# Optimization experiments

Hardware: AMD Instinct MI355X
Metric: run time of the kernel (lower is better)

Reference implementation:

```python
import jax, jax.numpy as jnp
import numpy as np
from jax import lax

DIM = 192
HID = 768  # dim * mlp_ratio
B, H, W = 16, 64, 64


def setup_inputs() -> dict:
    key = jax.random.key(0)
    ks = jax.random.split(key, 20)
    n = lambda k, shape, s=0.05: jax.random.normal(k, shape, dtype=jnp.float32) * s
    return {
        "x": jax.random.normal(ks[0], (B, DIM, H, W), dtype=jnp.float32),
        "ln1_w": jnp.ones((DIM,), jnp.float32), "ln1_b": jnp.zeros((DIM,), jnp.float32),
        "in_proj_w": n(ks[1], (2 * DIM, DIM)), "in_proj_b": n(ks[2], (2 * DIM,)),
        "dw_k": n(ks[3], (DIM, 1, 3, 3)),
        "le_k": n(ks[4], (DIM, 1, 3, 3)),
        "decay_logits": n(ks[5], (4, DIM), 0.5),
        "mix_logits": n(ks[6], (4, DIM), 0.5),
        "input_scale": n(ks[7], (4, DIM), 0.5),
        "bn_w": jnp.ones((DIM,), jnp.float32), "bn_b": jnp.zeros((DIM,), jnp.float32),
        "out_proj_w": n(ks[8], (DIM, DIM)), "out_proj_b": n(ks[9], (DIM,)),
        "ln2_w": jnp.ones((DIM,), jnp.float32), "ln2_b": jnp.zeros((DIM,), jnp.float32),
        "fc1_w": n(ks[10], (HID, DIM)), "fc1_b": n(ks[11], (HID,)),
        "fc2_w": n(ks[12], (DIM, HID)), "fc2_b": n(ks[13], (DIM,)),
    }


def _ln2d(x, w, b, eps=1e-6):
    # LayerNorm over channel dim of NCHW
    mean = jnp.mean(x, axis=1, keepdims=True)
    var = jnp.mean((x - mean) ** 2, axis=1, keepdims=True)
    xn = (x - mean) / jnp.sqrt(var + eps)
    return xn * w[None, :, None, None] + b[None, :, None, None]


def _conv1x1(x, w, b):
    return jnp.einsum('bchw,oc->bohw', x, w) + b[None, :, None, None]


def _dwconv3(x, k):
    # depthwise 3x3, padding=1; k: (C,1,3,3)
    return lax.conv_general_dilated(x, k, (1, 1), 'SAME',
                                    feature_group_count=x.shape[1],
                                    dimension_numbers=('NCHW', 'OIHW', 'NCHW'))


def _scan_axis(x, decay, axis):
    # linear decay scan along `axis` (-1 width, -2 height)
    xs = jnp.moveaxis(x, axis, 0)  # (L, B, C, ...)
    d = decay[None, :, None]  # broadcast over (B, C, other_spatial)
    def step(s, cur):
        s = d * s + (1.0 - d) * cur
        return s, s
    _, ys = lax.scan(step, jnp.zeros_like(xs[0]), xs)
    return jnp.moveaxis(ys, 0, axis)


def _directional_scan(x, decay_logits, mix_logits, input_scale):
    decay = jnp.clip(jax.nn.sigmoid(decay_logits), 0.05, 0.995)  # (4,C)
    mix = jax.nn.softmax(mix_logits, axis=0)  # (4,C)
    iscale = 1.0 + jnp.tanh(input_scale)  # (4,C)
    sc = lambda a: a[:, None, None]  # (C,1,1) -> broadcast NCHW
    lr = _scan_axis(x * sc(iscale[0]), decay[0], -1)
    rl = jnp.flip(_scan_axis(jnp.flip(x, -1) * sc(iscale[1]), decay[1], -1), -1)
    tb = _scan_axis(x * sc(iscale[2]), decay[2], -2)
    bt = jnp.flip(_scan_axis(jnp.flip(x, -2) * sc(iscale[3]), decay[3], -2), -2)
    return sc(mix[0]) * lr + sc(mix[1]) * rl + sc(mix[2]) * tb + sc(mix[3]) * bt


def reference(x, ln1_w, ln1_b, in_proj_w, in_proj_b, dw_k, le_k,
              decay_logits, mix_logits, input_scale, bn_w, bn_b,
              out_proj_w, out_proj_b, ln2_w, ln2_b, fc1_w, fc1_b, fc2_w, fc2_b):
    # --- SSM branch ---
    h = _ln2d(x, ln1_w, ln1_b)
    pg = _conv1x1(h, in_proj_w, in_proj_b)
    projected, gate = jnp.split(pg, 2, axis=1)
    projected = _dwconv3(projected, dw_k)
    scanned = _directional_scan(projected, decay_logits, mix_logits, input_scale)
    local = _dwconv3(projected, le_k)
    mixed = (scanned + local) * jax.nn.sigmoid(gate)
    # BatchNorm2d (training-mode batch statistics, eps=1e-5)
    bmean = jnp.mean(mixed, axis=(0, 2, 3), keepdims=True)
    bvar = jnp.mean((mixed - bmean) ** 2, axis=(0, 2, 3), keepdims=True)
    bn = (mixed - bmean) / jnp.sqrt(bvar + 1e-5)
    bn = bn * bn_w[None, :, None, None] + bn_b[None, :, None, None]
    mixed = jax.nn.gelu(bn, approximate=False)
    x = x + _conv1x1(mixed, out_proj_w, out_proj_b)
    # --- MLP branch ---
    h2 = _ln2d(x, ln2_w, ln2_b)
    m = jax.nn.gelu(_conv1x1(h2, fc1_w, fc1_b), approximate=False)
    m = _conv1x1(m, fc2_w, fc2_b)
    return x + m
```

## Files before the change

### kernel.cpp

```cpp
#include <hip/hip_runtime.h>
#include <math.h>

#define CH 192
#define HW 4096
#define NB 16
#define NELEM (NB*CH*HW)
#define HIDN 768

typedef __bf16 bf16x8 __attribute__((ext_vector_type(8)));
typedef float  f32x4  __attribute__((ext_vector_type(4)));
typedef unsigned uint4v __attribute__((ext_vector_type(4)));

__device__ __forceinline__ float gelu_f(float v){
    return v / (1.0f + __expf(-1.702f*v));
}
__device__ __forceinline__ float sigmoid_f(float v){
    return 1.0f / (1.0f + __expf(-v));
}
__device__ __forceinline__ void gload16(const void* g, void* l){
    __builtin_amdgcn_global_load_lds(
        (const __attribute__((address_space(1))) unsigned*)g,
        (__attribute__((address_space(3))) unsigned*)l, 16, 0, 0);
}

__global__ __launch_bounds__(256) void k_cvt_all(
    const float* __restrict__ a0, const float* __restrict__ a1,
    const float* __restrict__ a2, const float* __restrict__ a3,
    __bf16* __restrict__ o)
{
    const int n0 = 2*CH*CH, n1 = CH*CH, n2 = HIDN*CH, n3 = CH*HIDN;
    int i = blockIdx.x*256 + threadIdx.x;
    if (i < n0) o[i] = (__bf16)a0[i];
    else if (i < n0+n1) o[i] = (__bf16)a1[i-n0];
    else if (i < n0+n1+n2) o[i] = (__bf16)a2[i-n0-n1];
    else if (i < n0+n1+n2+n3) o[i] = (__bf16)a3[i-n0-n1-n2];
}

__global__ __launch_bounds__(256, 4) void k_ln_inproj(
    const float* __restrict__ x, const float* __restrict__ lw, const float* __restrict__ lb,
    const __bf16* __restrict__ Wb, const float* __restrict__ bias,
    __bf16* __restrict__ proj, __bf16* __restrict__ gate)
{
    __shared__ __align__(16) unsigned char smem[33792];
    __bf16* h2s = (__bf16*)smem;
    float* redS = (float*)(smem + 24576);
    float* redQ = (float*)(smem + 25600);
    float* mS   = (float*)(smem + 26624);
    float* rS   = (float*)(smem + 26880);
    __bf16* outb = (__bf16*)(smem + 24576);

    int tid = threadIdx.x;
    int lane = tid & 63;
    int w = tid >> 6;
    int lo = lane & 15, hi = lane >> 4;
    int bid = blockIdx.x;
    int b = bid >> 6;
    int p0 = (bid & 63) << 6;
    const float* xb = x + (size_t)b*CH*HW + p0;
    int px = lane;

    float xv[48];
    float s = 0.f, s2 = 0.f;
    #pragma unroll
    for (int k = 0; k < 48; ++k){
        float v = xb[(size_t)(48*w + k)*HW + px];
        xv[k] = v; s += v; s2 += v*v;
    }
    redS[tid] = s; redQ[tid] = s2;
    __syncthreads();
    if (tid < 64){
        float S = redS[tid]+redS[tid+64]+redS[tid+128]+redS[tid+192];
        float Q = redQ[tid]+redQ[tid+64]+redQ[tid+128]+redQ[tid+192];
        float mean = S * (1.f/192.f);
        float var  = Q * (1.f/192.f) - mean*mean;
        mS[tid] = mean;
        rS[tid] = rsqrtf(var + 1e-6f);
    }
    __syncthreads();
    {
        float mean = mS[px], rstd = rS[px];
        #pragma unroll
        for (int m = 0; m < 6; ++m){
            int c8 = 48*w + 8*m;
            int ks = c8 >> 5, hh = (c8 >> 3) & 3;
            bf16x8 pk;
            #pragma unroll
            for (int j = 0; j < 8; ++j){
                int c = c8 + j;
                pk[j] = (__bf16)((xv[8*m + j] - mean) * rstd * lw[c] + lb[c]);
            }
            *(bf16x8*)(h2s + (((px>>4)*6 + ks)*64 + hh*16 + (px & 15))*8) = pk;
        }
    }
    __syncthreads();

    #pragma unroll
    for (int g = 0; g < 2; ++g){
        f32x4 acc[3][4];
        #pragma unroll
        for (int nt = 0; nt < 3; ++nt)
            #pragma unroll
            for (int pt = 0; pt < 4; ++pt)
                acc[nt][pt] = (f32x4){0.f,0.f,0.f,0.f};
        #pragma unroll
        for (int ks = 0; ks < 6; ++ks){
            bf16x8 a[4];
            #pragma unroll
            for (int pt = 0; pt < 4; ++pt)
                a[pt] = *(const bf16x8*)(h2s + ((pt*6 + ks)*64 + lane)*8);
            #pragma unroll
            for (int nt = 0; nt < 3; ++nt){
                bf16x8 bf = *(const bf16x8*)
                    (Wb + (size_t)(g*192 + w*48 + nt*16 + lo)*CH + ks*32 + hi*8);
                #pragma unroll
                for (int pt = 0; pt < 4; ++pt)
                    acc[nt][pt] = __builtin_amdgcn_mfma_f32_16x16x32_bf16(
                        a[pt], bf, acc[nt][pt], 0, 0, 0);
            }
        }
        __bf16* dst = (g == 0) ? proj : gate;
        #pragma unroll
        for (int nt = 0; nt < 3; ++nt){
            __syncthreads();
            int oc = w*48 + nt*16 + lo;
            float bv = bias[g*CH + oc];
            int cc = w*16 + lo;
            #pragma unroll
            for (int pt = 0; pt < 4; ++pt)
                #pragma unroll
                for (int r = 0; r < 4; ++r){
                    float v = acc[nt][pt][r] + bv;
                    if (g == 1) v = sigmoid_f(v);
                    outb[cc*72 + pt*16 + hi*4 + r] = (__bf16)v;
                }
            __syncthreads();
            #pragma unroll
            for (int k = 0; k < 2; ++k){
                int i = tid + k*256;
                int c2 = i >> 3, vg = i & 7;
                int c = (c2 >> 4)*48 + nt*16 + (c2 & 15);
                bf16x8 o8 = *(const bf16x8*)(outb + c2*72 + vg*8);
                *(bf16x8*)(dst + (size_t)(b*CH + c)*HW + p0 + vg*8) = o8;
            }
        }
        __syncthreads();
    }
}

__global__ __launch_bounds__(256, 4) void k_spatial(
    const __bf16* __restrict__ proj, const __bf16* __restrict__ gate,
    const float* __restrict__ dwk, const float* __restrict__ lek,
    const float* __restrict__ dl, const float* __restrict__ ml, const float* __restrict__ il,
    __bf16* __restrict__ mixed, float* __restrict__ part)
{
    __shared__ float t[66*67];
    __shared__ __bf16 r[64*65];
    __shared__ __bf16 r2[64*65];
    __shared__ float rs[256], rq[256];
    int tid = threadIdx.x;
    int lane = tid & 63;
    int w = tid >> 6;
    int bc = blockIdx.x;
    int c = bc % CH;
    const __bf16* pp = proj + (size_t)bc*HW;

    for (int i = tid; i < 66*67; i += 256) t[i] = 0.f;
    float d[4], e[4], m[4];
    {
        float lg[4], mx = -1e30f;
        #pragma unroll
        for (int k = 0; k < 4; ++k){ lg[k] = ml[k*CH + c]; mx = fmaxf(mx, lg[k]); }
        float se = 0.f;
        #pragma unroll
        for (int k = 0; k < 4; ++k){ lg[k] = __expf(lg[k]-mx); se += lg[k]; }
        #pragma unroll
        for (int k = 0; k < 4; ++k){
            m[k] = lg[k] / se;
            float dd = sigmoid_f(dl[k*CH + c]);
            dd = fminf(fmaxf(dd, 0.05f), 0.995f);
            d[k] = dd;
            e[k] = (1.0f - dd) * (1.0f + tanhf(il[k*CH + c]));
        }
    }
    __syncthreads();
    #pragma unroll
    for (int k = 0; k < 2; ++k){
        int i = tid + k*256;
        int y = i >> 3, vg = i & 7;
        bf16x8 p8 = *(const bf16x8*)(pp + y*64 + vg*8);
        #pragma unroll
        for (int j = 0; j < 8; ++j)
            t[(y+1)*67 + vg*8 + j + 1] = (float)p8[j];
    }
    __syncthreads();
    float kk[9];
    #pragma unroll
    for (int j = 0; j < 9; ++j) kk[j] = dwk[c*9 + j];
    float dw[16];
    #pragma unroll
    for (int j = 0; j < 16; ++j){
        int i = tid + j*256;
        int y = i >> 6, xx = i & 63;
        float sv = 0.f;
        #pragma unroll
        for (int dy = 0; dy < 3; ++dy)
            #pragma unroll
            for (int dx = 0; dx < 3; ++dx)
                sv = fmaf(kk[dy*3+dx], t[(y+dy)*67 + xx + dx], sv);
        dw[j] = sv;
    }
    __syncthreads();
    #pragma unroll
    for (int j = 0; j < 16; ++j){
        int i = tid + j*256;
        t[((i>>6)+1)*67 + (i & 63) + 1] = dw[j];
    }
    __syncthreads();
    if (w == 0){
        int y = lane; float s = 0.f;
        for (int xx = 0; xx < 64; ++xx){
            s = fmaf(d[0], s, e[0]*t[(y+1)*67 + xx + 1]);
            r[y*65 + xx] = (__bf16)(m[0]*s);
        }
    } else if (w == 1){
        int xx = lane; float s = 0.f;
        for (int y = 0; y < 64; ++y){
            s = fmaf(d[2], s, e[2]*t[(y+1)*67 + xx + 1]);
            r2[y*65 + xx] = (__bf16)(m[2]*s);
        }
    }
    __syncthreads();
    if (w == 2){
        int y = lane; float s = 0.f;
        for (int xx = 63; xx >= 0; --xx){
            s = fmaf(d[1], s, e[1]*t[(y+1)*67 + xx + 1]);
            r[y*65 + xx] = (__bf16)((float)r[y*65 + xx] + m[1]*s);
        }
    } else if (w == 3){
        int xx = lane; float s = 0.f;
        for (int y = 63; y >= 0; --y){
            s = fmaf(d[3], s, e[3]*t[(y+1)*67 + xx + 1]);
            r2[y*65 + xx] = (__bf16)((float)r2[y*65 + xx] + m[3]*s);
        }
    }
    __syncthreads();
    float lk[9];
    #pragma unroll
    for (int j = 0; j < 9; ++j) lk[j] = lek[c*9 + j];
    const __bf16* gp = gate + (size_t)bc*HW;
    __bf16* mp = mixed + (size_t)bc*HW;
    float s1 = 0.f, s2 = 0.f;
    #pragma unroll
    for (int k = 0; k < 2; ++k){
        int i = tid + k*256;
        int y = i >> 3, vg = i & 7;
        bf16x8 g8 = *(const bf16x8*)(gp + y*64 + vg*8);
        bf16x8 m8;
        #pragma unroll
        for (int j = 0; j < 8; ++j){
            int xx = vg*8 + j;
            float sv = 0.f;
            #pragma unroll
            for (int dy = 0; dy < 3; ++dy)
                #pragma unroll
                for (int dx = 0; dx < 3; ++dx)
                    sv = fmaf(lk[dy*3+dx], t[(y+dy)*67 + xx + dx], sv);
            float mv = ((float)r[y*65 + xx] + (float)r2[y*65 + xx] + sv) * (float)g8[j];
            m8[j] = (__bf16)mv;
            s1 += mv; s2 += mv*mv;
        }
        *(bf16x8*)(mp + y*64 + vg*8) = m8;
    }
    rs[tid] = s1; rq[tid] = s2;
    __syncthreads();
    for (int off = 128; off > 0; off >>= 1){
        if (tid < off){ rs[tid] += rs[tid+off]; rq[tid] += rq[tid+off]; }
        __syncthreads();
    }
    if (tid == 0){ part[bc] = rs[0]; part[NB*CH + bc] = rq[0]; }
}

__global__ __launch_bounds__(192) void k_bn_final(
    const float* __restrict__ part, const float* __restrict__ bw,
    const float* __restrict__ bb, float* __restrict__ bnp)
{
    int c = threadIdx.x;
    float S = 0.f, Q = 0.f;
    for (int b = 0; b < NB; ++b){
        S += part[b*CH + c];
        Q += part[NB*CH + b*CH + c];
    }
    float mean = S * (1.f/65536.f);
    float var  = Q * (1.f/65536.f) - mean*mean;
    float sc = bw[c] * rsqrtf(var + 1e-5f);
    bnp[c] = sc;
    bnp[CH + c] = bb[c] - mean * sc;
}

__global__ __launch_bounds__(256, 4) void k_outproj_ln2(
    const __bf16* __restrict__ mixed, const float* __restrict__ bnp,
    const __bf16* __restrict__ Wo, const float* __restrict__ biaso,
    const float* __restrict__ x,
    const float* __restrict__ lw, const float* __restrict__ lb,
    float* __restrict__ xr, __bf16* __restrict__ ln2h)
{
    __shared__ __align__(16) unsigned char smem[27904];
    __bf16* h2s  = (__bf16*)smem;
    __bf16* outb = (__bf16*)smem;
    float* redS = (float*)(smem + 25344);
    float* redQ = (float*)(smem + 26368);
    float* mS   = (float*)(smem + 27392);
    float* rS   = (float*)(smem + 27648);

    int tid = threadIdx.x;
    int lane = tid & 63;
    int w = tid >> 6;
    int lo = lane & 15, hi = lane >> 4;
    int bid = blockIdx.x;
    int b = bid >> 6;
    int p0 = (bid & 63) << 6;
    int px = lane;
    const __bf16* mb = mixed + (size_t)b*CH*HW + p0;

    #pragma unroll
    for (int k = 0; k < 6; ++k){
        int V = tid + k*256;
        int c = V >> 3, vg = V & 7;
        bf16x8 m8 = *(const bf16x8*)(mb + (size_t)c*HW + vg*8);
        int ks = c >> 5, hh = (c >> 3) & 3, j2 = c & 7;
        float sc_ = bnp[c], sh_ = bnp[CH + c];
        #pragma unroll
        for (int j = 0; j < 8; ++j){
            int p2 = vg*8 + j;
            float v = gelu_f(fmaf((float)m8[j], sc_, sh_));
            h2s[((((p2>>4)*6 + ks) << 6) + hh*16 + (p2 & 15))*8 + j2] = (__bf16)v;
        }
    }
    __syncthreads();

    f32x4 acc[3][4];
    #pragma unroll
    for (int nt = 0; nt < 3; ++nt)
        #pragma unroll
        for (int pt = 0; pt < 4; ++pt)
            acc[nt][pt] = (f32x4){0.f,0.f,0.f,0.f};
    #pragma unroll
    for (int ks = 0; ks < 6; ++ks){
        bf16x8 a[4];
        #pragma unroll
        for (int pt = 0; pt < 4; ++pt)
            a[pt] = *(const bf16x8*)(h2s + ((pt*6 + ks)*64 + lane)*8);
        #pragma unroll
        for (int nt = 0; nt < 3; ++nt){
            bf16x8 bf = *(const bf16x8*)
                (Wo + (size_t)(w*48 + nt*16 + lo)*CH + ks*32 + hi*8);
            #pragma unroll
            for (int pt = 0; pt < 4; ++pt)
                acc[nt][pt] = __builtin_amdgcn_mfma_f32_16x16x32_bf16(
                    a[pt], bf, acc[nt][pt], 0, 0, 0);
        }
    }
    __syncthreads();

    #pragma unroll
    for (int nt = 0; nt < 3; ++nt){
        int ocl = w*48 + nt*16 + lo;
        #pragma unroll
        for (int pt = 0; pt < 4; ++pt)
            #pragma unroll
            for (int r = 0; r < 4; ++r)
                outb[ocl*66 + pt*16 + hi*4 + r] = (__bf16)acc[nt][pt][r];
    }
    __syncthreads();

    const float* xbb = x + (size_t)b*CH*HW + p0;
    float xv[48];
    float s = 0.f, s2 = 0.f;
    #pragma unroll
    for (int k = 0; k < 48; ++k){
        int c = 48*w + k;
        float v = xbb[(size_t)c*HW + px] + biaso[c] + (float)outb[c*66 + px];
        xv[k] = v; s += v; s2 += v*v;
    }
    redS[tid] = s; redQ[tid] = s2;
    __syncthreads();
    if (tid < 64){
        float S = redS[tid]+redS[tid+64]+redS[tid+128]+redS[tid+192];
        float Q = redQ[tid]+redQ[tid+64]+redQ[tid+128]+redQ[tid+192];
        float mean = S * (1.f/192.f);
        float var  = Q * (1.f/192.f) - mean*mean;
        mS[tid] = mean;
        rS[tid] = rsqrtf(var + 1e-6f);
    }
    __syncthreads();

    float* xrb = xr + (size_t)b*CH*HW + p0;
    {
        float mean = mS[px], rstd = rS[px];
        #pragma unroll
        for (int m = 0; m < 6; ++m){
            int c8 = 48*w + 8*m;
            int ks = c8 >> 5, hh = (c8 >> 3) & 3;
            bf16x8 pk;
            #pragma unroll
            for (int j = 0; j < 8; ++j){
                int c = c8 + j;
                float v = xv[8*m + j];
                xrb[(size_t)c*HW + px] = v;
                pk[j] = (__bf16)((v - mean) * rstd * lw[c] + lb[c]);
            }
            *(bf16x8*)(h2s + (((px>>4)*6 + ks)*64 + hh*16 + (px & 15))*8) = pk;
        }
    }
    __syncthreads();

    {
        uint4v* gdst = (uint4v*)(ln2h + (size_t)bid*12288);
        const uint4v* lsrc = (const uint4v*)h2s;
        #pragma unroll
        for (int k = 0; k < 6; ++k){
            int i = tid + k*256;
            gdst[i] = lsrc[i];
        }
    }
}

__global__ __launch_bounds__(256, 4) void k_mlp2(
    const __bf16* __restrict__ ln2h,
    const __bf16* __restrict__ w1b, const float* __restrict__ b1,
    const __bf16* __restrict__ w2b, const float* __restrict__ b2,
    float* __restrict__ io)
{
    __shared__ __align__(16) unsigned char smem[40960];
    __bf16* h2s = (__bf16*)smem;
    __bf16* tt0 = (__bf16*)(smem + 24576);
    __bf16* tt1 = (__bf16*)(smem + 32768);
    __bf16* outbb = (__bf16*)smem;

    int tid = threadIdx.x;
    int lane = tid & 63;
    int w = tid >> 6;
    int lo = lane & 15, hi = lane >> 4;
    int bid = blockIdx.x;
    int b = bid >> 6;
    int p0 = (bid & 63) << 6;

    {
        const unsigned char* src = (const unsigned char*)(ln2h + (size_t)bid*12288);
        #pragma unroll
        for (int k = 0; k < 6; ++k){
            int off = (tid + k*256)*16;
            gload16(src + off, smem + off);
        }
    }
    __syncthreads();

    f32x4 acc2[3][4];
    #pragma unroll
    for (int nt2 = 0; nt2 < 3; ++nt2)
        #pragma unroll
        for (int pt = 0; pt < 4; ++pt)
            acc2[nt2][pt] = (f32x4){0.f,0.f,0.f,0.f};

    int ks2c = w >> 1;
    int hi2c = 2*(w & 1) + (hi >> 1);
    int jbase = (hi & 1)*4;

    #pragma unroll 1
    for (int hc = 0; hc < 12; ++hc){
        int hb = hc*64;
        __bf16* ttw = (hc & 1) ? tt1 : tt0;
        f32x4 acc1[4];
        #pragma unroll
        for (int pt = 0; pt < 4; ++pt)
            acc1[pt] = (f32x4){0.f,0.f,0.f,0.f};
        #pragma unroll
        for (int ks = 0; ks < 6; ++ks){
            bf16x8 wf = *(const bf16x8*)
                (w1b + (size_t)(hb + w*16 + lo)*CH + ks*32 + hi*8);
            #pragma unroll
            for (int pt = 0; pt < 4; ++pt){
                bf16x8 a = *(const bf16x8*)(h2s + ((pt*6 + ks)*64 + lane)*8);
                acc1[pt] = __builtin_amdgcn_mfma_f32_16x16x32_bf16(
                    wf, a, acc1[pt], 0, 0, 0);
            }
        }
        {
            f32x4 bv4 = *(const f32x4*)(b1 + hb + w*16 + hi*4);
            #pragma unroll
            for (int pt = 0; pt < 4; ++pt){
                union { __bf16 h[4]; double d; } pk;
                #pragma unroll
                for (int r = 0; r < 4; ++r)
                    pk.h[r] = (__bf16)gelu_f(acc1[pt][r] + bv4[r]);
                *(double*)(ttw + ((pt*2 + ks2c)*64 + hi2c*16 + lo)*8 + jbase) = pk.d;
            }
        }
        __syncthreads();
        #pragma unroll
        for (int ks2 = 0; ks2 < 2; ++ks2){
            bf16x8 a2[4];
            #pragma unroll
            for (int pt = 0; pt < 4; ++pt)
                a2[pt] = *(const bf16x8*)(ttw + ((pt*2 + ks2)*64 + lane)*8);
            #pragma unroll
            for (int nt2 = 0; nt2 < 3; ++nt2){
                bf16x8 bf2 = *(const bf16x8*)
                    (w2b + (size_t)(w*48 + nt2*16 + lo)*HIDN + hb + ks2*32 + hi*8);
                #pragma unroll
                for (int pt = 0; pt < 4; ++pt)
                    acc2[nt2][pt] = __builtin_amdgcn_mfma_f32_16x16x32_bf16(
                        a2[pt], bf2, acc2[nt2][pt], 0, 0, 0);
            }
        }
    }
    __syncthreads();

    #pragma unroll
    for (int nt2 = 0; nt2 < 3; ++nt2){
        int ocl = w*48 + nt2*16 + lo;
        #pragma unroll
        for (int pt = 0; pt < 4; ++pt)
            #pragma unroll
            for (int r = 0; r < 4; ++r)
                outbb[ocl*72 + pt*16 + hi*4 + r] = (__bf16)acc2[nt2][pt][r];
    }
    __syncthreads();
    float* iob = io + (size_t)b*CH*HW + p0;
    #pragma unroll
    for (int k = 0; k < 6; ++k){
        int V = tid + k*256;
        int c = V >> 3, vg = V & 7;
        bf16x8 o8 = *(const bf16x8*)(outbb + c*72 + vg*8);
        float bv = b2[c];
        float* pr = iob + (size_t)c*HW + vg*8;
        f32x4 r0 = *(const f32x4*)pr;
        f32x4 r1 = *(const f32x4*)(pr + 4);
        #pragma unroll
        for (int j = 0; j < 4; ++j){
            r0[j] += bv + (float)o8[j];
            r1[j] += bv + (float)o8[4 + j];
        }
        *(f32x4*)pr = r0;
        *(f32x4*)(pr + 4) = r1;
    }
}

extern "C" void kernel_launch(void* const* d_in, const int* in_sizes, int n_in,
                              void* d_out, int out_size, void* d_ws, size_t ws_size,
                              hipStream_t stream) {
    const float* x    = (const float*)d_in[0];
    const float* ln1w = (const float*)d_in[1];
    const float* ln1b = (const float*)d_in[2];
    const float* ipw  = (const float*)d_in[3];
    const float* ipb  = (const float*)d_in[4];
    const float* dwk  = (const float*)d_in[5];
    const float* lek  = (const float*)d_in[6];
    const float* dlg  = (const float*)d_in[7];
    const float* mlg  = (const float*)d_in[8];
    const float* isc  = (const float*)d_in[9];
    const float* bnw  = (const float*)d_in[10];
    const float* bnb  = (const float*)d_in[11];
    const float* opw  = (const float*)d_in[12];
    const float* opb  = (const float*)d_in[13];
    const float* ln2w = (const float*)d_in[14];
    const float* ln2b = (const float*)d_in[15];
    const float* f1w  = (const float*)d_in[16];
    const float* f1b  = (const float*)d_in[17];
    const float* f2w  = (const float*)d_in[18];
    const float* f2b  = (const float*)d_in[19];

    float* out = (float*)d_out;
    __bf16* bufP = (__bf16*)d_ws;
    __bf16* bufG = bufP + (size_t)NELEM;
    __bf16* bufM = bufG + (size_t)NELEM;
    __bf16* ln2h = bufM + (size_t)NELEM;
    float* part = (float*)(ln2h + (size_t)NELEM);
    float* bnp  = part + 2*NB*CH;
    __bf16* ipwb = (__bf16*)(bnp + 2*CH);
    __bf16* opwb = ipwb + (size_t)2*CH*CH;
    __bf16* w1b  = opwb + (size_t)CH*CH;
    __bf16* w2b  = w1b  + (size_t)HIDN*CH;

    const int ncvt = 2*CH*CH + CH*CH + 2*HIDN*CH;
    k_cvt_all<<<(ncvt + 255)/256, 256, 0, stream>>>(ipw, opw, f1w, f2w, ipwb);

    k_ln_inproj  <<<1024, 256, 0, stream>>>(x, ln1w, ln1b, ipwb, ipb, bufP, bufG);
    k_spatial    <<<NB*CH, 256, 0, stream>>>(bufP, bufG, dwk, lek, dlg, mlg, isc, bufM, part);
    k_bn_final   <<<1, 192, 0, stream>>>(part, bnw, bnb, bnp);
    k_outproj_ln2<<<1024, 256, 0, stream>>>(bufM, bnp, opwb, opb, x, ln2w, ln2b, out, ln2h);
    k_mlp2       <<<1024, 256, 0, stream>>>(ln2h, w1b, f1b, w2b, f2b, out);
}
```

Before: 212.7 us.

## Fuse out-projection/LN2 kernel with MLP kernel, keep residual in registers

Result: faster. 203.0 us (-4.6%).

```diff
diff --git a/kernel.cpp b/kernel.cpp
--- a/kernel.cpp
+++ b/kernel.cpp
@@ -17,10 +17,9 @@
 __device__ __forceinline__ float sigmoid_f(float v){
     return 1.0f / (1.0f + __expf(-v));
 }
-__device__ __forceinline__ void gload16(const void* g, void* l){
-    __builtin_amdgcn_global_load_lds(
-        (const __attribute__((address_space(1))) unsigned*)g,
-        (__attribute__((address_space(3))) unsigned*)l, 16, 0, 0);
+__device__ __forceinline__ unsigned pack2bf(float a, float b){
+    union { __bf16 h[2]; unsigned u; } v;
+    v.h[0] = (__bf16)a; v.h[1] = (__bf16)b; return v.u;
 }
 
 __global__ __launch_bounds__(256) void k_cvt_all(
@@ -297,20 +296,25 @@
     bnp[CH + c] = bb[c] - mean * sc;
 }
 
-__global__ __launch_bounds__(256, 4) void k_outproj_ln2(
+__global__ __launch_bounds__(256, 4) void k_tail2(
     const __bf16* __restrict__ mixed, const float* __restrict__ bnp,
     const __bf16* __restrict__ Wo, const float* __restrict__ biaso,
     const float* __restrict__ x,
     const float* __restrict__ lw, const float* __restrict__ lb,
-    float* __restrict__ xr, __bf16* __restrict__ ln2h)
+    const __bf16* __restrict__ w1b, const float* __restrict__ b1,
+    const __bf16* __restrict__ w2b, const float* __restrict__ b2,
+    float* __restrict__ outp)
 {
-    __shared__ __align__(16) unsigned char smem[27904];
-    __bf16* h2s  = (__bf16*)smem;
-    __bf16* outb = (__bf16*)smem;
-    float* redS = (float*)(smem + 25344);
-    float* redQ = (float*)(smem + 26368);
-    float* mS   = (float*)(smem + 27392);
-    float* rS   = (float*)(smem + 27648);
+    __shared__ __align__(16) unsigned char smem[40960];
+    __bf16* h2s = (__bf16*)smem;
+    __bf16* tt0 = (__bf16*)(smem + 24576);
+    __bf16* tt1 = (__bf16*)(smem + 32768);
+    __bf16* outb66 = (__bf16*)smem;
+    float* redS = (float*)(smem + 25600);
+    float* redQ = (float*)(smem + 26624);
+    float* mS   = (float*)(smem + 27648);
+    float* rS   = (float*)(smem + 27904);
+    float* outf = (float*)smem;
 
     int tid = threadIdx.x;
     int lane = tid & 63;
@@ -338,64 +342,64 @@
     }
     __syncthreads();
 
-    f32x4 acc[3][4];
-    #pragma unroll
-    for (int nt = 0; nt < 3; ++nt)
-        #pragma unroll
-        for (int pt = 0; pt < 4; ++pt)
-            acc[nt][pt] = (f32x4){0.f,0.f,0.f,0.f};
-    #pragma unroll
-    for (int ks = 0; ks < 6; ++ks){
-        bf16x8 a[4];
-        #pragma unroll
-        for (int pt = 0; pt < 4; ++pt)
-            a[pt] = *(const bf16x8*)(h2s + ((pt*6 + ks)*64 + lane)*8);
+    {
+        f32x4 acc[3][4];
+        #pragma unroll
+        for (int nt = 0; nt < 3; ++nt)
+            #pragma unroll
+            for (int pt = 0; pt < 4; ++pt)
+                acc[nt][pt] = (f32x4){0.f,0.f,0.f,0.f};
+        #pragma unroll
+        for (int ks = 0; ks < 6; ++ks){
+            bf16x8 a[4];
+            #pragma unroll
+            for (int pt = 0; pt < 4; ++pt)
+                a[pt] = *(const bf16x8*)(h2s + ((pt*6 + ks)*64 + lane)*8);
+            #pragma unroll
+            for (int nt = 0; nt < 3; ++nt){
+                bf16x8 bf = *(const bf16x8*)
+                    (Wo + (size_t)(w*48 + nt*16 + lo)*CH + ks*32 + hi*8);
+                #pragma unroll
+                for (int pt = 0; pt < 4; ++pt)
+                    acc[nt][pt] = __builtin_amdgcn_mfma_f32_16x16x32_bf16(
+                        a[pt], bf, acc[nt][pt], 0, 0, 0);
+            }
+        }
+        __syncthreads();
         #pragma unroll
         for (int nt = 0; nt < 3; ++nt){
-            bf16x8 bf = *(const bf16x8*)
-                (Wo + (size_t)(w*48 + nt*16 + lo)*CH + ks*32 + hi*8);
-            #pragma unroll
-            for (int pt = 0; pt < 4; ++pt)
-                acc[nt][pt] = __builtin_amdgcn_mfma_f32_16x16x32_bf16(
-                    a[pt], bf, acc[nt][pt], 0, 0, 0);
-        }
-    }
-    __syncthreads();
-
-    #pragma unroll
-    for (int nt = 0; nt < 3; ++nt){
-        int ocl = w*48 + nt*16 + lo;
-        #pragma unroll
-        for (int pt = 0; pt < 4; ++pt)
-            #pragma unroll
-            for (int r = 0; r < 4; ++r)
-                outb[ocl*66 + pt*16 + hi*4 + r] = (__bf16)acc[nt][pt][r];
-    }
-    __syncthreads();
-
-    const float* xbb = x + (size_t)b*CH*HW + p0;
-    float xv[48];
-    float s = 0.f, s2 = 0.f;
-    #pragma unroll
-    for (int k = 0; k < 48; ++k){
-        int c = 48*w + k;
-        float v = xbb[(size_t)c*HW + px] + biaso[c] + (float)outb[c*66 + px];
-        xv[k] = v; s += v; s2 += v*v;
-    }
-    redS[tid] = s; redQ[tid] = s2;
-    __syncthreads();
-    if (tid < 64){
-        float S = redS[tid]+redS[tid+64]+redS[tid+128]+redS[tid+192];
-        float Q = redQ[tid]+redQ[tid+64]+redQ[tid+128]+redQ[tid+192];
-        float mean = S * (1.f/192.f);
-        float var  = Q * (1.f/192.f) - mean*mean;
-        mS[tid] = mean;
-        rS[tid] = rsqrtf(var + 1e-6f);
-    }
-    __syncthreads();
-
-    float* xrb = xr + (size_t)b*CH*HW + p0;
+            int ocl = w*48 + nt*16 + lo;
+            #pragma unroll
+            for (int pt = 0; pt < 4; ++pt)
+                #pragma unroll
+                for (int r = 0; r < 4; ++r)
+                    outb66[ocl*66 + pt*16 + hi*4 + r] = (__bf16)acc[nt][pt][r];
+        }
+    }
+    __syncthreads();
+
+    unsigned xp[24];
     {
+        const float* xbb = x + (size_t)b*CH*HW + p0;
+        float xv[48];
+        float s = 0.f, s2 = 0.f;
+        #pragma unroll
+        for (int k = 0; k < 48; ++k){
+            int c = 48*w + k;
+            float v = xbb[(size_t)c*HW + px] + biaso[c] + (float)outb66[c*66 + px];
+            xv[k] = v; s += v; s2 += v*v;
+        }
+        redS[tid] = s; redQ[tid] = s2;
+        __syncthreads();
+        if (tid < 64){
+            float S = redS[tid]+redS[tid+64]+redS[tid+128]+redS[tid+192];
+            float Q = redQ[tid]+redQ[tid+64]+redQ[tid+128]+redQ[tid+192];
+            float mean = S * (1.f/192.f);
+            float var  = Q * (1.f/192.f) - mean*mean;
+            mS[tid] = mean;
+            rS[tid] = rsqrtf(var + 1e-6f);
+        }
+        __syncthreads();
         float mean = mS[px], rstd = rS[px];
         #pragma unroll
         for (int m = 0; m < 6; ++m){
@@ -405,53 +409,13 @@
             #pragma unroll
             for (int j = 0; j < 8; ++j){
                 int c = c8 + j;
-                float v = xv[8*m + j];
-                xrb[(size_t)c*HW + px] = v;
-                pk[j] = (__bf16)((v - mean) * rstd * lw[c] + lb[c]);
+                pk[j] = (__bf16)((xv[8*m + j] - mean) * rstd * lw[c] + lb[c]);
             }
             *(bf16x8*)(h2s + (((px>>4)*6 + ks)*64 + hh*16 + (px & 15))*8) = pk;
         }
-    }
-    __syncthreads();
-
-    {
-        uint4v* gdst = (uint4v*)(ln2h + (size_t)bid*12288);
-        const uint4v* lsrc = (const uint4v*)h2s;
-        #pragma unroll
-        for (int k = 0; k < 6; ++k){
-            int i = tid + k*256;
-            gdst[i] = lsrc[i];
-        }
-    }
-}
-
-__global__ __launch_bounds__(256, 4) void k_mlp2(
-    const __bf16* __restrict__ ln2h,
-    const __bf16* __restrict__ w1b, const float* __restrict__ b1,
-    const __bf16* __restrict__ w2b, const float* __restrict__ b2,
-    float* __restrict__ io)
-{
-    __shared__ __align__(16) unsigned char smem[40960];
-    __bf16* h2s = (__bf16*)smem;
-    __bf16* tt0 = (__bf16*)(smem + 24576);
-    __bf16* tt1 = (__bf16*)(smem + 32768);
-    __bf16* outbb = (__bf16*)smem;
-
-    int tid = threadIdx.x;
-    int lane = tid & 63;
-    int w = tid >> 6;
-    int lo = lane & 15, hi = lane >> 4;
-    int bid = blockIdx.x;
-    int b = bid >> 6;
-    int p0 = (bid & 63) << 6;
-
-    {
-        const unsigned char* src = (const unsigned char*)(ln2h + (size_t)bid*12288);
-        #pragma unroll
-        for (int k = 0; k < 6; ++k){
-            int off = (tid + k*256)*16;
-            gload16(src + off, smem + off);
-        }
+        #pragma unroll
+        for (int k2 = 0; k2 < 24; ++k2)
+            xp[k2] = pack2bf(xv[2*k2], xv[2*k2+1]);
     }
     __syncthreads();
 
@@ -516,33 +480,46 @@
     }
     __syncthreads();
 
-    #pragma unroll
-    for (int nt2 = 0; nt2 < 3; ++nt2){
-        int ocl = w*48 + nt2*16 + lo;
-        #pragma unroll
-        for (int pt = 0; pt < 4; ++pt)
-            #pragma unroll
-            for (int r = 0; r < 4; ++r)
-                outbb[ocl*72 + pt*16 + hi*4 + r] = (__bf16)acc2[nt2][pt][r];
-    }
-    __syncthreads();
-    float* iob = io + (size_t)b*CH*HW + p0;
-    #pragma unroll
-    for (int k = 0; k < 6; ++k){
-        int V = tid + k*256;
-        int c = V >> 3, vg = V & 7;
-        bf16x8 o8 = *(const bf16x8*)(outbb + c*72 + vg*8);
-        float bv = b2[c];
-        float* pr = iob + (size_t)c*HW + vg*8;
-        f32x4 r0 = *(const f32x4*)pr;
-        f32x4 r1 = *(const f32x4*)(pr + 4);
-        #pragma unroll
-        for (int j = 0; j < 4; ++j){
-            r0[j] += bv + (float)o8[j];
-            r1[j] += bv + (float)o8[4 + j];
-        }
-        *(f32x4*)pr = r0;
-        *(f32x4*)(pr + 4) = r1;
+    float* iob = outp + (size_t)b*CH*HW + p0;
+    #pragma unroll
+    for (int half = 0; half < 2; ++half){
+        if ((w >> 1) == half){
+            #pragma unroll
+            for (int nt2 = 0; nt2 < 3; ++nt2){
+                int cl = (w & 1)*48 + nt2*16 + lo;
+                #pragma unroll
+                for (int pt = 0; pt < 4; ++pt)
+                    #pragma unroll
+                    for (int r = 0; r < 4; ++r)
+                        outf[cl*68 + pt*16 + hi*4 + r] = acc2[nt2][pt][r];
+            }
+        }
+        __syncthreads();
+        if ((w >> 1) == half){
+            #pragma unroll
+            for (int k = 0; k < 48; ++k){
+                int cl = (w & 1)*48 + k;
+                union { unsigned u; float f; } vv;
+                unsigned bits = (k & 1) ? (xp[k>>1] >> 16) : (xp[k>>1] & 0xffffu);
+                vv.u = bits << 16;
+                outf[cl*68 + px] += vv.f;
+            }
+        }
+        __syncthreads();
+        #pragma unroll
+        for (int k = 0; k < 3; ++k){
+            int V = tid + k*256;
+            int cl = V >> 3, vg = V & 7;
+            int c = half*96 + cl;
+            f32x4 r0 = *(const f32x4*)(outf + cl*68 + vg*8);
+            f32x4 r1 = *(const f32x4*)(outf + cl*68 + vg*8 + 4);
+            float bv = b2[c];
+            #pragma unroll
+            for (int j = 0; j < 4; ++j){ r0[j] += bv; r1[j] += bv; }
+            *(f32x4*)(iob + (size_t)c*HW + vg*8) = r0;
+            *(f32x4*)(iob + (size_t)c*HW + vg*8 + 4) = r1;
+        }
+        __syncthreads();
     }
 }
 
@@ -574,8 +551,7 @@
     __bf16* bufP = (__bf16*)d_ws;
     __bf16* bufG = bufP + (size_t)NELEM;
     __bf16* bufM = bufG + (size_t)NELEM;
-    __bf16* ln2h = bufM + (size_t)NELEM;
-    float* part = (float*)(ln2h + (size_t)NELEM);
+    float* part = (float*)(bufM + (size_t)NELEM);
     float* bnp  = part + 2*NB*CH;
     __bf16* ipwb = (__bf16*)(bnp + 2*CH);
     __bf16* opwb = ipwb + (size_t)2*CH*CH;
@@ -585,9 +561,9 @@
     const int ncvt = 2*CH*CH + CH*CH + 2*HIDN*CH;
     k_cvt_all<<<(ncvt + 255)/256, 256, 0, stream>>>(ipw, opw, f1w, f2w, ipwb);
 
-    k_ln_inproj  <<<1024, 256, 0, stream>>>(x, ln1w, ln1b, ipwb, ipb, bufP, bufG);
-    k_spatial    <<<NB*CH, 256, 0, stream>>>(bufP, bufG, dwk, lek, dlg, mlg, isc, bufM, part);
-    k_bn_final   <<<1, 192, 0, stream>>>(part, bnw, bnb, bnp);
-    k_outproj_ln2<<<1024, 256, 0, stream>>>(bufM, bnp, opwb, opb, x, ln2w, ln2b, out, ln2h);
-    k_mlp2       <<<1024, 256, 0, stream>>>(ln2h, w1b, f1b, w2b, f2b, out);
-}
+    k_ln_inproj<<<1024, 256, 0, stream>>>(x, ln1w, ln1b, ipwb, ipb, bufP, bufG);
+    k_spatial  <<<NB*CH, 256, 0, stream>>>(bufP, bufG, dwk, lek, dlg, mlg, isc, bufM, part);
+    k_bn_final <<<1, 192, 0, stream>>>(part, bnw, bnb, bnp);
+    k_tail2    <<<1024, 256, 0, stream>>>(bufM, bnp, opwb, opb, x, ln2w, ln2b,
+                                          w1b, f1b, w2b, f2b, out);
+}
```
